# Kernel optimization log

Hardware: AMD Instinct MI355X
Metric: run time of the kernel (lower is better)

The kernel has to match this reference:

```python
import jax, jax.numpy as jnp
import numpy as np

N_NODES = 100000
N_EDGES = 3200000
HIDDEN = 128


def _linear_params(key, din, dout):
    s = 1.0 / np.sqrt(din)
    kw, kb = jax.random.split(key)
    W = jax.random.uniform(kw, (dout, din), minval=-s, maxval=s, dtype=jnp.float32)
    b = jax.random.uniform(kb, (dout,), minval=-s, maxval=s, dtype=jnp.float32)
    return W, b


def setup_inputs() -> dict:
    key = jax.random.key(0)
    ks = jax.random.split(key, 9)
    x = jax.random.normal(ks[0], (N_NODES, 5), dtype=jnp.float32)
    edge_index = jax.random.randint(ks[1], (2, N_EDGES), 0, N_NODES, dtype=jnp.int64)
    W1, b1 = _linear_params(ks[2], 5, 64)
    W2, b2 = _linear_params(ks[3], 64, HIDDEN)
    W3, b3 = _linear_params(ks[4], HIDDEN, HIDDEN)
    W4, b4 = _linear_params(ks[5], HIDDEN, HIDDEN)
    Wc1, bc1 = _linear_params(ks[6], HIDDEN, HIDDEN)
    Wc2, bc2 = _linear_params(ks[7], HIDDEN, HIDDEN)
    W5, b5 = _linear_params(ks[8], HIDDEN, 60)
    return {"x": x, "edge_index": edge_index,
            "W1": W1, "b1": b1, "W2": W2, "b2": b2,
            "W3": W3, "b3": b3, "W4": W4, "b4": b4,
            "Wc1": Wc1, "bc1": bc1, "Wc2": Wc2, "bc2": bc2,
            "W5": W5, "b5": b5}


def gcn_conv(x, edge_index, W, b):
    """GCNConv: self-loops + symmetric deg^-1/2 normalization."""
    n = x.shape[0]
    loop = jnp.arange(n, dtype=edge_index.dtype)
    src = jnp.concatenate([edge_index[0], loop])  # [E+N]
    dst = jnp.concatenate([edge_index[1], loop])  # [E+N]
    h = x @ W.T                                    # [N, H]
    ones = jnp.ones_like(dst, dtype=h.dtype)
    deg = jax.ops.segment_sum(ones, dst, num_segments=n)         # [N]
    dinv = jnp.where(deg > 0, jax.lax.rsqrt(deg), 0.0)
    norm = dinv[src] * dinv[dst]                                  # [E+N]
    msg = h[src] * norm[:, None]                                  # gather + scale
    out = jax.ops.segment_sum(msg, dst, num_segments=n)           # scatter-add
    return out + b


def reference(x, edge_index, W1, b1, W2, b2, W3, b3, W4, b4,
              Wc1, bc1, Wc2, bc2, W5, b5):
    h = jax.nn.relu(x @ W1.T + b1)
    h = jax.nn.relu(h @ W2.T + b2)
    h = jax.nn.relu(h @ W3.T + b3) + h
    h = jax.nn.relu(h @ W4.T + b4) + h
    h = jax.nn.relu(gcn_conv(h, edge_index, Wc1, bc1))
    h = jax.nn.relu(gcn_conv(h, edge_index, Wc2, bc2))
    return h @ W5.T + b5  # [N, 60]
```

## Files before the change

### kernel.cpp

```cpp
#include <hip/hip_runtime.h>
#include <hip/hip_fp16.h>

typedef __attribute__((ext_vector_type(8))) short bf16x8;
typedef __attribute__((ext_vector_type(4))) float f32x4;

__device__ __forceinline__ float frelu(float v){ return fmaxf(v, 0.f); }
__device__ __forceinline__ short f2bf(float f){
  unsigned u = __float_as_uint(f);
  unsigned r = (u + 0x7fffu + ((u>>16)&1u)) >> 16;
  return (short)r;
}
__device__ __forceinline__ float bf2f(short h){
  return __uint_as_float(((unsigned)(unsigned short)h) << 16);
}

template<int K, int BN, int COLS_REAL, int PRE, int EPI, int WRG, int WCG>
__global__ __launch_bounds__(512) void k_mgemm(const float* __restrict__ A,
    const float* __restrict__ W, const float* __restrict__ bpre,
    const float* __restrict__ bpost, const float* __restrict__ dscale,
    float* __restrict__ Out, int n)
{
  constexpr int BM = WRG*64;
  __shared__ __align__(16) short sAh[BM*32];
  __shared__ __align__(16) short sAl[BM*32];
  __shared__ __align__(16) short sWh[BN*32];
  __shared__ __align__(16) short sWl[BN*32];

  const int tid = threadIdx.x;
  const int nb0 = blockIdx.x * BM;
  const int l = tid & 63;
  const int w = tid >> 6;
  const int wr = w % WRG;
  const int wc = w / WRG;
  const int lrow = l & 15;
  const int koct = l >> 4;

  f32x4 acc[4][4];
  #pragma unroll
  for (int i=0;i<4;i++)
    #pragma unroll
    for (int j=0;j<4;j++) acc[i][j] = (f32x4){0.f,0.f,0.f,0.f};

  for (int kc = 0; kc < K/32; ++kc) {
    if (kc) __syncthreads();
    #pragma unroll
    for (int t = 0; t < BM/128; ++t) {
      int idx = tid + t*512;
      int row = idx >> 2, kq = idx & 3;
      int node = nb0 + row;
      float a[8];
      if (node < n) {
        const float* g = A + (size_t)node*K + kc*32 + kq*8;
        float4 v0 = *(const float4*)g;
        float4 v1 = *(const float4*)(g+4);
        a[0]=v0.x; a[1]=v0.y; a[2]=v0.z; a[3]=v0.w;
        a[4]=v1.x; a[5]=v1.y; a[6]=v1.z; a[7]=v1.w;
      } else {
        #pragma unroll
        for (int j=0;j<8;j++) a[j]=0.f;
      }
      if constexpr (PRE == 1) {
        const float* bp = bpre + kc*32 + kq*8;
        float4 b0 = *(const float4*)bp;
        float4 b1 = *(const float4*)(bp+4);
        a[0]=frelu(a[0]+b0.x); a[1]=frelu(a[1]+b0.y);
        a[2]=frelu(a[2]+b0.z); a[3]=frelu(a[3]+b0.w);
        a[4]=frelu(a[4]+b1.x); a[5]=frelu(a[5]+b1.y);
        a[6]=frelu(a[6]+b1.z); a[7]=frelu(a[7]+b1.w);
      }
      union { short s[8]; bf16x8 v; } ph, pl;
      #pragma unroll
      for (int j=0;j<8;j++) {
        short h = f2bf(a[j]);
        ph.s[j] = h;
        pl.s[j] = f2bf(a[j] - bf2f(h));
      }
      int byte = (row<<6) | (kq<<4);
      byte ^= (row&7)<<4;
      *(bf16x8*)((char*)sAh + byte) = ph.v;
      *(bf16x8*)((char*)sAl + byte) = pl.v;
    }
    if (BN*4 >= 512 || tid < BN*4) {
      int idx = tid;
      int c = idx >> 2, kq = idx & 3;
      float a[8];
      if (COLS_REAL == BN || c < COLS_REAL) {
        const float* g = W + (size_t)c*K + kc*32 + kq*8;
        float4 v0 = *(const float4*)g;
        float4 v1 = *(const float4*)(g+4);
        a[0]=v0.x; a[1]=v0.y; a[2]=v0.z; a[3]=v0.w;
        a[4]=v1.x; a[5]=v1.y; a[6]=v1.z; a[7]=v1.w;
      } else {
        #pragma unroll
        for (int j=0;j<8;j++) a[j]=0.f;
      }
      union { short s[8]; bf16x8 v; } ph, pl;
      #pragma unroll
      for (int j=0;j<8;j++) {
        short h = f2bf(a[j]);
        ph.s[j] = h;
        pl.s[j] = f2bf(a[j] - bf2f(h));
      }
      int byte = (c<<6) | (kq<<4);
      byte ^= (c&7)<<4;
      *(bf16x8*)((char*)sWh + byte) = ph.v;
      *(bf16x8*)((char*)sWl + byte) = pl.v;
    }
    __syncthreads();
    bf16x8 fah[4], fal[4], fwh[4], fwl[4];
    #pragma unroll
    for (int rf=0; rf<4; ++rf) {
      int row = wr*64 + rf*16 + lrow;
      int byte = (row<<6) | (koct<<4);
      byte ^= (row&7)<<4;
      fah[rf] = *(const bf16x8*)((const char*)sAh + byte);
      fal[rf] = *(const bf16x8*)((const char*)sAl + byte);
    }
    #pragma unroll
    for (int cf=0; cf<4; ++cf) {
      int c = wc*64 + cf*16 + lrow;
      int byte = (c<<6) | (koct<<4);
      byte ^= (c&7)<<4;
      fwh[cf] = *(const bf16x8*)((const char*)sWh + byte);
      fwl[cf] = *(const bf16x8*)((const char*)sWl + byte);
    }
    #pragma unroll
    for (int rf=0; rf<4; ++rf)
      #pragma unroll
      for (int cf=0; cf<4; ++cf) {
        acc[rf][cf] = __builtin_amdgcn_mfma_f32_16x16x32_bf16(fah[rf], fwh[cf], acc[rf][cf], 0,0,0);
        acc[rf][cf] = __builtin_amdgcn_mfma_f32_16x16x32_bf16(fah[rf], fwl[cf], acc[rf][cf], 0,0,0);
        acc[rf][cf] = __builtin_amdgcn_mfma_f32_16x16x32_bf16(fal[rf], fwh[cf], acc[rf][cf], 0,0,0);
      }
  }
  const int crow = (l >> 4) * 4;
  float bpc[4];
  if constexpr (EPI==1 || EPI==2 || EPI==3) {
    #pragma unroll
    for (int cf=0; cf<4; ++cf) {
      int col = wc*64 + cf*16 + (l & 15);
      bpc[cf] = (COLS_REAL == BN || col < COLS_REAL) ? bpost[col] : 0.f;
    }
  }
  #pragma unroll
  for (int rf=0; rf<4; ++rf) {
    #pragma unroll
    for (int reg=0; reg<4; ++reg) {
      int row = wr*64 + rf*16 + crow + reg;
      int node = nb0 + row;
      if (node >= n) continue;
      float ds = 1.f;
      if constexpr (EPI==4 || EPI==5) ds = dscale[node];
      #pragma unroll
      for (int cf=0; cf<4; ++cf) {
        int col = wc*64 + cf*16 + (l & 15);
        if (COLS_REAL != BN && col >= COLS_REAL) continue;
        float v = acc[rf][cf][reg];
        if constexpr (EPI==1) v += bpc[cf];
        if constexpr (EPI==2) v = frelu(v + bpc[cf]);
        if constexpr (EPI==3) v = frelu(v + bpc[cf]) + A[(size_t)node*K + col];
        if constexpr (EPI==4) v *= ds;
        if constexpr (EPI==5) {
          v *= ds;
          ((__half*)Out)[(size_t)node*COLS_REAL + col] = __float2half_rn(v);
        } else {
          Out[(size_t)node*COLS_REAL + col] = v;
        }
      }
    }
  }
}

__global__ __launch_bounds__(256) void k_wsplit(const float* __restrict__ W2,
    const float* __restrict__ W3, const float* __restrict__ W4,
    const float* __restrict__ Wc1, short* __restrict__ whi, short* __restrict__ wlo)
{
  int idx = blockIdx.x*256 + threadIdx.x;
  if (idx >= 57344) return;
  const float* src; int e, c, k, cbase;
  if (idx < 8192){ src=W2; e=idx; c=e>>6; k=e&63; cbase=0; }
  else if (idx < 24576){ src=W3; e=idx-8192; c=e>>7; k=e&127; cbase=8192; }
  else if (idx < 40960){ src=W4; e=idx-24576; c=e>>7; k=e&127; cbase=24576; }
  else { src=Wc1; e=idx-40960; c=e>>7; k=e&127; cbase=40960; }
  float v = src[e];
  short h = f2bf(v);
  short lo = f2bf(v - bf2f(h));
  int byte = ((c<<6) | ((k&31)<<1)) ^ ((c&7)<<4);
  int pos = cbase + (k>>5)*4096 + (byte>>1);
  whi[pos] = h; wlo[pos] = lo;
}

__global__ __launch_bounds__(256) void k_mega(const float* __restrict__ x,
    const float* __restrict__ W1, const float* __restrict__ b1,
    const float* __restrict__ b2, const float* __restrict__ b3,
    const float* __restrict__ b4, const short* __restrict__ whi,
    const short* __restrict__ wlo, const float* __restrict__ dinv,
    __half* __restrict__ tp1, int n)
{
  __shared__ __align__(16) short sWh[4096], sWl[4096];
  __shared__ __align__(16) short bAh[4096], bAl[4096];
  __shared__ __align__(16) short bBh[4096], bBl[4096];
  __shared__ float sx[160];
  __shared__ float sW1[320];
  __shared__ float sb1[64];
  const int tid = threadIdx.x;
  const int nb0 = blockIdx.x*32;

  if (tid < 160){ int row = tid/5, col = tid - row*5; int node = nb0 + row;
    sx[tid] = (node < n) ? x[(size_t)node*5 + col] : 0.f; }
  if (tid < 64) sb1[tid] = b1[tid];
  for (int i = tid; i < 320; i += 256) sW1[i] = W1[i];
  __syncthreads();

  {
    int row = tid >> 3, c0 = (tid & 7)*8;
    float xr[5];
    #pragma unroll
    for (int k=0;k<5;k++) xr[k] = sx[row*5+k];
    #pragma unroll
    for (int j=0;j<8;j++){
      int c = c0 + j;
      float a = sb1[c];
      #pragma unroll
      for (int k=0;k<5;k++) a = fmaf(xr[k], sW1[c*5+k], a);
      a = frelu(a);
      short h = f2bf(a), lo = f2bf(a - bf2f(h));
      int byte = ((c>>5)<<11) + ((((row<<6)|((c&31)<<1))) ^ ((row&7)<<4));
      *(short*)((char*)bAh + byte) = h;
      *(short*)((char*)bAl + byte) = lo;
    }
  }

  const int l = tid & 63, w = tid >> 6;
  const int wr = w >> 1, wc = w & 1;
  const int lrow = l & 15, koct = l >> 4;
  const int arow = wr*16 + lrow;
  const int abyteNoKc = ((arow<<6)|(koct<<4)) ^ ((arow&7)<<4);
  int wbyte[4];
  #pragma unroll
  for (int cf=0; cf<4; ++cf){
    int c = wc*64 + cf*16 + lrow;
    wbyte[cf] = ((c<<6)|(koct<<4)) ^ ((c&7)<<4);
  }
  f32x4 acc[4];
  float res[4][4];

  auto run_layer = [&](const short* inH, const short* inL, int woff, int nkc){
    #pragma unroll
    for (int cf=0; cf<4; ++cf) acc[cf] = (f32x4){0.f,0.f,0.f,0.f};
    for (int kc=0; kc<nkc; ++kc){
      __syncthreads();
      {
        const bf16x8* gh = (const bf16x8*)(whi + woff + kc*4096);
        const bf16x8* gl = (const bf16x8*)(wlo + woff + kc*4096);
        ((bf16x8*)sWh)[tid*2]   = gh[tid*2];
        ((bf16x8*)sWh)[tid*2+1] = gh[tid*2+1];
        ((bf16x8*)sWl)[tid*2]   = gl[tid*2];
        ((bf16x8*)sWl)[tid*2+1] = gl[tid*2+1];
      }
      __syncthreads();
      int ab = (kc<<11) + abyteNoKc;
      bf16x8 fah = *(const bf16x8*)((const char*)inH + ab);
      bf16x8 fal = *(const bf16x8*)((const char*)inL + ab);
      #pragma unroll
      for (int cf=0; cf<4; ++cf){
        bf16x8 fwh = *(const bf16x8*)((const char*)sWh + wbyte[cf]);
        bf16x8 fwl = *(const bf16x8*)((const char*)sWl + wbyte[cf]);
        acc[cf] = __builtin_amdgcn_mfma_f32_16x16x32_bf16(fah, fwh, acc[cf], 0,0,0);
        acc[cf] = __builtin_amdgcn_mfma_f32_16x16x32_bf16(fah, fwl, acc[cf], 0,0,0);
        acc[cf] = __builtin_amdgcn_mfma_f32_16x16x32_bf16(fal, fwh, acc[cf], 0,0,0);
      }
    }
  };
  auto store_buf = [&](short* outH, short* outL, int cf, int reg, float v){
    int row = wr*16 + koct*4 + reg;
    int col = wc*64 + cf*16 + lrow;
    short h = f2bf(v), lo = f2bf(v - bf2f(h));
    int byte = ((col>>5)<<11) + (((row<<6)|((col&31)<<1)) ^ ((row&7)<<4));
    *(short*)((char*)outH + byte) = h;
    *(short*)((char*)outL + byte) = lo;
  };

  run_layer(bAh, bAl, 0, 2);
  #pragma unroll
  for (int cf=0; cf<4; ++cf){
    float bb = b2[wc*64 + cf*16 + lrow];
    #pragma unroll
    for (int reg=0; reg<4; ++reg){
      float v = frelu(acc[cf][reg] + bb);
      res[cf][reg] = v;
      store_buf(bBh, bBl, cf, reg, v);
    }
  }
  run_layer(bBh, bBl, 8192, 4);
  #pragma unroll
  for (int cf=0; cf<4; ++cf){
    float bb = b3[wc*64 + cf*16 + lrow];
    #pragma unroll
    for (int reg=0; reg<4; ++reg){
      float v = frelu(acc[cf][reg] + bb) + res[cf][reg];
      res[cf][reg] = v;
      store_buf(bAh, bAl, cf, reg, v);
    }
  }
  run_layer(bAh, bAl, 24576, 4);
  #pragma unroll
  for (int cf=0; cf<4; ++cf){
    float bb = b4[wc*64 + cf*16 + lrow];
    #pragma unroll
    for (int reg=0; reg<4; ++reg){
      float v = frelu(acc[cf][reg] + bb) + res[cf][reg];
      store_buf(bBh, bBl, cf, reg, v);
    }
  }
  run_layer(bBh, bBl, 40960, 4);
  #pragma unroll
  for (int reg=0; reg<4; ++reg){
    int row = wr*16 + koct*4 + reg;
    int node = nb0 + row;
    float di = dinv[min(node, n-1)];
    #pragma unroll
    for (int cf=0; cf<4; ++cf){
      int col = wc*64 + cf*16 + lrow;
      if (node < n) tp1[(size_t)node*128 + col] = __float2half_rn(acc[cf][reg]*di);
    }
  }
}

__global__ __launch_bounds__(512) void k_zero512(int* __restrict__ a, int m){
  int i = threadIdx.x; if (i<m) a[i]=0;
}
__global__ __launch_bounds__(512) void k_bhist(const int* __restrict__ dst,
    int* __restrict__ bcnt, int E, int nbuck){
  __shared__ int l[512];
  int tid = threadIdx.x;
  if (tid < nbuck) l[tid]=0;
  __syncthreads();
  for (int e = blockIdx.x*512 + tid; e < E; e += gridDim.x*512)
    atomicAdd(&l[((unsigned)dst[e])>>8], 1);
  __syncthreads();
  if (tid < nbuck && l[tid]) atomicAdd(&bcnt[tid], l[tid]);
}
__global__ __launch_bounds__(512) void k_bscan(const int* __restrict__ bcnt,
    int* __restrict__ bbase, int* __restrict__ bcur, int nbuck){
  __shared__ int sc[512];
  int tid = threadIdx.x;
  int v = (tid<nbuck) ? bcnt[tid] : 0;
  sc[tid]=v; __syncthreads();
  for (int off=1; off<512; off<<=1){
    int t = (tid>=off)? sc[tid-off] : 0;
    __syncthreads();
    sc[tid]+=t;
    __syncthreads();
  }
  if (tid<nbuck){ bbase[tid]=sc[tid]-v; bcur[tid]=sc[tid]-v; }
  if (tid==nbuck-1) bbase[nbuck]=sc[tid];
}
__global__ __launch_bounds__(512) void k_bscatter(const int* __restrict__ src,
    const int* __restrict__ dst, int* __restrict__ bcur,
    unsigned* __restrict__ sorted, int E, int nbuck)
{
  __shared__ int lcnt[512];
  __shared__ int lbase[512];
  int tid = threadIdx.x;
  if (tid < nbuck) lcnt[tid]=0;
  __syncthreads();
  int e0 = blockIdx.x*8192;
  int e1 = min(e0+8192, E);
  for (int e = e0+tid; e < e1; e += 512)
    atomicAdd(&lcnt[((unsigned)dst[e])>>8], 1);
  __syncthreads();
  if (tid < nbuck) lbase[tid] = lcnt[tid] ? atomicAdd(&bcur[tid], lcnt[tid]) : 0;
  __syncthreads();
  if (tid < nbuck) lcnt[tid]=0;
  __syncthreads();
  for (int e = e0+tid; e < e1; e += 512){
    int d = dst[e];
    int k = ((unsigned)d)>>8;
    int pos = lbase[k] + atomicAdd(&lcnt[k], 1);
    sorted[pos] = (((unsigned)src[e])<<8) | ((unsigned)d & 255u);
  }
}
__global__ __launch_bounds__(512) void k_finesort(unsigned* __restrict__ sorted,
    const int* __restrict__ bbase, int* __restrict__ cend,
    float* __restrict__ dinv, int n, int* __restrict__ fb)
{
  constexpr int CAP = 16384;
  __shared__ int lsorted[CAP];
  __shared__ int cnt[256], cur[256], sc[256];
  const int k = blockIdx.x;
  const int base = bbase[k], endb = bbase[k+1];
  const int m = endb - base;
  const int node0 = k<<8;
  const int tid = threadIdx.x;
  if (tid<256) cnt[tid]=0;
  __syncthreads();
  for (int i=tid; i<m; i+=512) atomicAdd(&cnt[sorted[base+i]&255u], 1);
  __syncthreads();
  int v=0;
  if (tid<256){ v=cnt[tid]; sc[tid]=v; }
  __syncthreads();
  for (int off=1; off<256; off<<=1){
    int t=0;
    if (tid>=off && tid<256) t=sc[tid-off];
    __syncthreads();
    if (tid<256) sc[tid]+=t;
    __syncthreads();
  }
  if (tid<256){
    cur[tid]=sc[tid]-v;
    int node = node0 + tid;
    if (node < n){
      cend[node] = base + sc[tid];
      dinv[node] = rsqrtf((float)v + 1.0f);
    }
  }
  __syncthreads();
  if (m <= CAP){
    for (int i=tid; i<m; i+=512){
      unsigned p = sorted[base+i];
      int pos = atomicAdd(&cur[p&255u], 1);
      lsorted[pos] = (int)(p>>8);
    }
    __syncthreads();
    for (int i=tid; i<m; i+=512) sorted[base+i] = (unsigned)lsorted[i];
  } else {
    for (int i=tid; i<m; i+=512) fb[base+i] = (int)sorted[base+i];
    __syncthreads();
    for (int i=tid; i<m; i+=512){
      unsigned p = (unsigned)fb[base+i];
      int pos = atomicAdd(&cur[p&255u], 1);
      sorted[base+pos] = p>>8;
    }
  }
}

__global__ __launch_bounds__(256) void k_agg(const int* __restrict__ cend,
    const unsigned* __restrict__ srcs, const float* __restrict__ dinv,
    const __half* __restrict__ tp, float* __restrict__ out, int n)
{
  int node = blockIdx.x*4 + (threadIdx.x>>6);
  if (node >= n) return;
  const int lane = threadIdx.x & 63;
  const __half2* tpp = (const __half2*)tp;
  int beg = (node==0) ? 0 : cend[node-1];
  int end = cend[node];
  float2 acc;
  { __half2 h = tpp[(size_t)node*64 + lane]; acc.x = __low2float(h); acc.y = __high2float(h); }
  int e = beg;
  for (; e+4<=end; e+=4){
    unsigned s0=srcs[e], s1=srcs[e+1], s2=srcs[e+2], s3=srcs[e+3];
    __half2 h0 = tpp[(size_t)s0*64 + lane];
    __half2 h1 = tpp[(size_t)s1*64 + lane];
    __half2 h2 = tpp[(size_t)s2*64 + lane];
    __half2 h3 = tpp[(size_t)s3*64 + lane];
    acc.x += (__low2float(h0)+__low2float(h1)) + (__low2float(h2)+__low2float(h3));
    acc.y += (__high2float(h0)+__high2float(h1)) + (__high2float(h2)+__high2float(h3));
  }
  for (; e<end; ++e){
    __half2 h = tpp[(size_t)srcs[e]*64 + lane];
    acc.x += __low2float(h); acc.y += __high2float(h);
  }
  float di = dinv[node];
  float2 r; r.x = acc.x*di; r.y = acc.y*di;
  *(float2*)(out + (size_t)node*128 + (lane<<1)) = r;
}

extern "C" void kernel_launch(void* const* d_in, const int* in_sizes, int n_in,
                              void* d_out, int out_size, void* d_ws, size_t ws_size,
                              hipStream_t stream)
{
  const float* x   = (const float*)d_in[0];
  const int*   ei  = (const int*)d_in[1];
  const float *W1=(const float*)d_in[2],  *b1=(const float*)d_in[3];
  const float *W2=(const float*)d_in[4],  *b2=(const float*)d_in[5];
  const float *W3=(const float*)d_in[6],  *b3=(const float*)d_in[7];
  const float *W4=(const float*)d_in[8],  *b4=(const float*)d_in[9];
  const float *Wc1=(const float*)d_in[10],*bc1=(const float*)d_in[11];
  const float *Wc2=(const float*)d_in[12],*bc2=(const float*)d_in[13];
  const float *W5=(const float*)d_in[14], *b5=(const float*)d_in[15];
  float* out = (float*)d_out;

  const int n = in_sizes[0] / 5;
  const int E = in_sizes[1] / 2;
  const int* esrc = ei;
  const int* edst = ei + E;
  const int nbuck = (n + 255) >> 8;

  dim3 B256(256), B512(512);
  const int G256 = (n + 255)/256;
  const int G512 = (n + 511)/512;

  char* p = (char*)d_ws;
  float* hA    = (float*)p;           p += (size_t)n*128*4;
  float* hB    = (float*)p;           p += (size_t)n*128*4;
  float* dinv  = (float*)p;           p += (size_t)n*4;
  int*   cend  = (int*)p;             p += (size_t)n*4;
  unsigned* sortedp = (unsigned*)p;   p += (size_t)E*4;
  int*   bcnt  = (int*)p;             p += 512*4;
  int*   bbase = (int*)p;             p += 513*4;
  int*   bcur  = (int*)p;             p += 512*4;
  short* whi   = (short*)p;           p += 57344*2;
  short* wlo   = (short*)p;           p += 57344*2;

  k_zero512<<<dim3(1), B512, 0, stream>>>(bcnt, nbuck);
  k_bhist<<<dim3(512), B512, 0, stream>>>(edst, bcnt, E, nbuck);
  k_bscan<<<dim3(1), B512, 0, stream>>>(bcnt, bbase, bcur, nbuck);
  k_bscatter<<<dim3((E + 8191)/8192), B512, 0, stream>>>(esrc, edst, bcur, sortedp, E, nbuck);
  k_finesort<<<dim3(nbuck), B512, 0, stream>>>(sortedp, bbase, cend, dinv, n, (int*)hA);

  k_wsplit<<<dim3(224), B256, 0, stream>>>(W2, W3, W4, Wc1, whi, wlo);

  k_mega<<<dim3((n + 31)/32), B256, 0, stream>>>(x, W1, b1, b2, b3, b4,
                                                 whi, wlo, dinv, (__half*)hA, n);
  k_agg<<<dim3((n+3)/4), B256, 0, stream>>>(cend, sortedp, dinv, (const __half*)hA, hB, n);

  k_mgemm<128,128,128,1,5,4,2><<<dim3(G256), B512, 0, stream>>>(hB, Wc2, bc1, nullptr, dinv, hA, n);
  k_agg<<<dim3((n+3)/4), B256, 0, stream>>>(cend, sortedp, dinv, (const __half*)hA, hB, n);

  k_mgemm<128,64,60,1,1,8,1><<<dim3(G512), B512, 0, stream>>>(hB, W5, bc2, b5, nullptr, out, n);
}
```

Before: 448.8 us.

## Store transformed features column-chunked and aggregate per 16-column chunk

The fp16 transformed features are now written in a chunk-major layout: 8 chunks of 16 columns, each stored contiguously across all nodes. The aggregation kernel gives each block one column chunk, so a chunk's gather working set is about 3.2 MB instead of the full 25.6 MB table, which should raise L2 hit rates. Within a wavefront, 8 edges are processed in parallel with 8 lanes per edge, and a shuffle reduction follows. In exchange, each gathered row segment is only 32 bytes, edge indices are re-read once per chunk (8x), and the tail iterations use masked loads.

After: 1.006 ms. 2.24x slower.

```diff
diff --git a/kernel.cpp b/kernel.cpp
--- a/kernel.cpp
+++ b/kernel.cpp
@@ -162,7 +162,7 @@
         if constexpr (EPI==4) v *= ds;
         if constexpr (EPI==5) {
           v *= ds;
-          ((__half*)Out)[(size_t)node*COLS_REAL + col] = __float2half_rn(v);
+          ((__half*)Out)[((size_t)(col>>4)*n + node)*16 + (col&15)] = __float2half_rn(v);
         } else {
           Out[(size_t)node*COLS_REAL + col] = v;
         }
@@ -322,7 +322,8 @@
     #pragma unroll
     for (int cf=0; cf<4; ++cf){
       int col = wc*64 + cf*16 + lrow;
-      if (node < n) tp1[(size_t)node*128 + col] = __float2half_rn(acc[cf][reg]*di);
+      if (node < n)
+        tp1[((size_t)(col>>4)*n + node)*16 + (col&15)] = __float2half_rn(acc[cf][reg]*di);
     }
   }
 }
@@ -435,35 +436,42 @@
   }
 }
 
-__global__ __launch_bounds__(256) void k_agg(const int* __restrict__ cend,
+__global__ __launch_bounds__(512) void k_aggc(const int* __restrict__ cend,
     const unsigned* __restrict__ srcs, const float* __restrict__ dinv,
     const __half* __restrict__ tp, float* __restrict__ out, int n)
 {
-  int node = blockIdx.x*4 + (threadIdx.x>>6);
+  const int chunk = blockIdx.x & 7;
+  const int node = (blockIdx.x >> 3)*8 + (threadIdx.x >> 6);
   if (node >= n) return;
-  const int lane = threadIdx.x & 63;
-  const __half2* tpp = (const __half2*)tp;
-  int beg = (node==0) ? 0 : cend[node-1];
-  int end = cend[node];
-  float2 acc;
-  { __half2 h = tpp[(size_t)node*64 + lane]; acc.x = __low2float(h); acc.y = __high2float(h); }
-  int e = beg;
-  for (; e+4<=end; e+=4){
-    unsigned s0=srcs[e], s1=srcs[e+1], s2=srcs[e+2], s3=srcs[e+3];
-    __half2 h0 = tpp[(size_t)s0*64 + lane];
-    __half2 h1 = tpp[(size_t)s1*64 + lane];
-    __half2 h2 = tpp[(size_t)s2*64 + lane];
-    __half2 h3 = tpp[(size_t)s3*64 + lane];
-    acc.x += (__low2float(h0)+__low2float(h1)) + (__low2float(h2)+__low2float(h3));
-    acc.y += (__high2float(h0)+__high2float(h1)) + (__high2float(h2)+__high2float(h3));
-  }
-  for (; e<end; ++e){
-    __half2 h = tpp[(size_t)srcs[e]*64 + lane];
+  const int l = threadIdx.x & 63;
+  const int eg = l >> 3, ch = l & 7;
+  const __half2* tpc = (const __half2*)tp + (size_t)chunk*n*8;
+  const int beg = (node==0) ? 0 : cend[node-1];
+  const int end = cend[node];
+  float2 acc = {0.f, 0.f};
+  const int iters = (end - beg + 7) >> 3;
+  for (int i=0; i<iters; ++i){
+    int e = beg + i*8 + eg;
+    int ec = min(e, end-1);
+    unsigned s = __builtin_nontemporal_load(srcs + ec);
+    __half2 h = tpc[(size_t)s*8 + ch];
+    float m = (e < end) ? 1.f : 0.f;
+    acc.x = fmaf(__low2float(h), m, acc.x);
+    acc.y = fmaf(__high2float(h), m, acc.y);
+  }
+  #pragma unroll
+  for (int msk=8; msk<64; msk<<=1){
+    acc.x += __shfl_xor(acc.x, msk, 64);
+    acc.y += __shfl_xor(acc.y, msk, 64);
+  }
+  if (eg == 0){
+    __half2 h = tpc[(size_t)node*8 + ch];
     acc.x += __low2float(h); acc.y += __high2float(h);
-  }
-  float di = dinv[node];
-  float2 r; r.x = acc.x*di; r.y = acc.y*di;
-  *(float2*)(out + (size_t)node*128 + (lane<<1)) = r;
+    float di = dinv[node];
+    float2 r; r.x = acc.x*di; r.y = acc.y*di;
+    double rb; __builtin_memcpy(&rb, &r, 8);
+    __builtin_nontemporal_store(rb, (double*)(out + (size_t)node*128 + (chunk*8+ch)*2));
+  }
 }
 
 extern "C" void kernel_launch(void* const* d_in, const int* in_sizes, int n_in,
@@ -490,6 +498,7 @@
   dim3 B256(256), B512(512);
   const int G256 = (n + 255)/256;
   const int G512 = (n + 511)/512;
+  const int GAGG = 8 * ((n + 7)/8);
 
   char* p = (char*)d_ws;
   float* hA    = (float*)p;           p += (size_t)n*128*4;
@@ -513,10 +522,10 @@
 
   k_mega<<<dim3((n + 31)/32), B256, 0, stream>>>(x, W1, b1, b2, b3, b4,
                                                  whi, wlo, dinv, (__half*)hA, n);
-  k_agg<<<dim3((n+3)/4), B256, 0, stream>>>(cend, sortedp, dinv, (const __half*)hA, hB, n);
+  k_aggc<<<dim3(GAGG), B512, 0, stream>>>(cend, sortedp, dinv, (const __half*)hA, hB, n);
 
   k_mgemm<128,128,128,1,5,4,2><<<dim3(G256), B512, 0, stream>>>(hB, Wc2, bc1, nullptr, dinv, hA, n);
-  k_agg<<<dim3((n+3)/4), B256, 0, stream>>>(cend, sortedp, dinv, (const __half*)hA, hB, n);
+  k_aggc<<<dim3(GAGG), B512, 0, stream>>>(cend, sortedp, dinv, (const __half*)hA, hB, n);
 
   k_mgemm<128,64,60,1,1,8,1><<<dim3(G512), B512, 0, stream>>>(hB, W5, bc2, b5, nullptr, out, n);
 }
```

## Fuse GCN aggregation with following dense GEMM into one kernel

Applied to the files above, without the earlier changes.

Replaces the separate aggregation kernel and split-bf16 GEMM pair with a single kernel. Each 512-thread block gathers neighbour rows for 128 nodes, applies the dinv scale, bias and ReLU, and writes the result as hi/lo bf16 into shared memory. It then runs the MFMA GEMM directly on that tile. This removes the fp32 round trip of the aggregated features through global memory. The cost is a large shared-memory tile that limits occupancy for the latency-bound gather phase, and the GEMM cannot start until the whole block's gather is done.

Measured after the change: 631.5 us. 1.41x slower.

```diff
diff --git a/kernel.cpp b/kernel.cpp
--- a/kernel.cpp
+++ b/kernel.cpp
@@ -12,163 +12,6 @@
 }
 __device__ __forceinline__ float bf2f(short h){
   return __uint_as_float(((unsigned)(unsigned short)h) << 16);
-}
-
-template<int K, int BN, int COLS_REAL, int PRE, int EPI, int WRG, int WCG>
-__global__ __launch_bounds__(512) void k_mgemm(const float* __restrict__ A,
-    const float* __restrict__ W, const float* __restrict__ bpre,
-    const float* __restrict__ bpost, const float* __restrict__ dscale,
-    float* __restrict__ Out, int n)
-{
-  constexpr int BM = WRG*64;
-  __shared__ __align__(16) short sAh[BM*32];
-  __shared__ __align__(16) short sAl[BM*32];
-  __shared__ __align__(16) short sWh[BN*32];
-  __shared__ __align__(16) short sWl[BN*32];
-
-  const int tid = threadIdx.x;
-  const int nb0 = blockIdx.x * BM;
-  const int l = tid & 63;
-  const int w = tid >> 6;
-  const int wr = w % WRG;
-  const int wc = w / WRG;
-  const int lrow = l & 15;
-  const int koct = l >> 4;
-
-  f32x4 acc[4][4];
-  #pragma unroll
-  for (int i=0;i<4;i++)
-    #pragma unroll
-    for (int j=0;j<4;j++) acc[i][j] = (f32x4){0.f,0.f,0.f,0.f};
-
-  for (int kc = 0; kc < K/32; ++kc) {
-    if (kc) __syncthreads();
-    #pragma unroll
-    for (int t = 0; t < BM/128; ++t) {
-      int idx = tid + t*512;
-      int row = idx >> 2, kq = idx & 3;
-      int node = nb0 + row;
-      float a[8];
-      if (node < n) {
-        const float* g = A + (size_t)node*K + kc*32 + kq*8;
-        float4 v0 = *(const float4*)g;
-        float4 v1 = *(const float4*)(g+4);
-        a[0]=v0.x; a[1]=v0.y; a[2]=v0.z; a[3]=v0.w;
-        a[4]=v1.x; a[5]=v1.y; a[6]=v1.z; a[7]=v1.w;
-      } else {
-        #pragma unroll
-        for (int j=0;j<8;j++) a[j]=0.f;
-      }
-      if constexpr (PRE == 1) {
-        const float* bp = bpre + kc*32 + kq*8;
-        float4 b0 = *(const float4*)bp;
-        float4 b1 = *(const float4*)(bp+4);
-        a[0]=frelu(a[0]+b0.x); a[1]=frelu(a[1]+b0.y);
-        a[2]=frelu(a[2]+b0.z); a[3]=frelu(a[3]+b0.w);
-        a[4]=frelu(a[4]+b1.x); a[5]=frelu(a[5]+b1.y);
-        a[6]=frelu(a[6]+b1.z); a[7]=frelu(a[7]+b1.w);
-      }
-      union { short s[8]; bf16x8 v; } ph, pl;
-      #pragma unroll
-      for (int j=0;j<8;j++) {
-        short h = f2bf(a[j]);
-        ph.s[j] = h;
-        pl.s[j] = f2bf(a[j] - bf2f(h));
-      }
-      int byte = (row<<6) | (kq<<4);
-      byte ^= (row&7)<<4;
-      *(bf16x8*)((char*)sAh + byte) = ph.v;
-      *(bf16x8*)((char*)sAl + byte) = pl.v;
-    }
-    if (BN*4 >= 512 || tid < BN*4) {
-      int idx = tid;
-      int c = idx >> 2, kq = idx & 3;
-      float a[8];
-      if (COLS_REAL == BN || c < COLS_REAL) {
-        const float* g = W + (size_t)c*K + kc*32 + kq*8;
-        float4 v0 = *(const float4*)g;
-        float4 v1 = *(const float4*)(g+4);
-        a[0]=v0.x; a[1]=v0.y; a[2]=v0.z; a[3]=v0.w;
-        a[4]=v1.x; a[5]=v1.y; a[6]=v1.z; a[7]=v1.w;
-      } else {
-        #pragma unroll
-        for (int j=0;j<8;j++) a[j]=0.f;
-      }
-      union { short s[8]; bf16x8 v; } ph, pl;
-      #pragma unroll
-      for (int j=0;j<8;j++) {
-        short h = f2bf(a[j]);
-        ph.s[j] = h;
-        pl.s[j] = f2bf(a[j] - bf2f(h));
-      }
-      int byte = (c<<6) | (kq<<4);
-      byte ^= (c&7)<<4;
-      *(bf16x8*)((char*)sWh + byte) = ph.v;
-      *(bf16x8*)((char*)sWl + byte) = pl.v;
-    }
-    __syncthreads();
-    bf16x8 fah[4], fal[4], fwh[4], fwl[4];
-    #pragma unroll
-    for (int rf=0; rf<4; ++rf) {
-      int row = wr*64 + rf*16 + lrow;
-      int byte = (row<<6) | (koct<<4);
-      byte ^= (row&7)<<4;
-      fah[rf] = *(const bf16x8*)((const char*)sAh + byte);
-      fal[rf] = *(const bf16x8*)((const char*)sAl + byte);
-    }
-    #pragma unroll
-    for (int cf=0; cf<4; ++cf) {
-      int c = wc*64 + cf*16 + lrow;
-      int byte = (c<<6) | (koct<<4);
-      byte ^= (c&7)<<4;
-      fwh[cf] = *(const bf16x8*)((const char*)sWh + byte);
-      fwl[cf] = *(const bf16x8*)((const char*)sWl + byte);
-    }
-    #pragma unroll
-    for (int rf=0; rf<4; ++rf)
-      #pragma unroll
-      for (int cf=0; cf<4; ++cf) {
-        acc[rf][cf] = __builtin_amdgcn_mfma_f32_16x16x32_bf16(fah[rf], fwh[cf], acc[rf][cf], 0,0,0);
-        acc[rf][cf] = __builtin_amdgcn_mfma_f32_16x16x32_bf16(fah[rf], fwl[cf], acc[rf][cf], 0,0,0);
-        acc[rf][cf] = __builtin_amdgcn_mfma_f32_16x16x32_bf16(fal[rf], fwh[cf], acc[rf][cf], 0,0,0);
-      }
-  }
-  const int crow = (l >> 4) * 4;
-  float bpc[4];
-  if constexpr (EPI==1 || EPI==2 || EPI==3) {
-    #pragma unroll
-    for (int cf=0; cf<4; ++cf) {
-      int col = wc*64 + cf*16 + (l & 15);
-      bpc[cf] = (COLS_REAL == BN || col < COLS_REAL) ? bpost[col] : 0.f;
-    }
-  }
-  #pragma unroll
-  for (int rf=0; rf<4; ++rf) {
-    #pragma unroll
-    for (int reg=0; reg<4; ++reg) {
-      int row = wr*64 + rf*16 + crow + reg;
-      int node = nb0 + row;
-      if (node >= n) continue;
-      float ds = 1.f;
-      if constexpr (EPI==4 || EPI==5) ds = dscale[node];
-      #pragma unroll
-      for (int cf=0; cf<4; ++cf) {
-        int col = wc*64 + cf*16 + (l & 15);
-        if (COLS_REAL != BN && col >= COLS_REAL) continue;
-        float v = acc[rf][cf][reg];
-        if constexpr (EPI==1) v += bpc[cf];
-        if constexpr (EPI==2) v = frelu(v + bpc[cf]);
-        if constexpr (EPI==3) v = frelu(v + bpc[cf]) + A[(size_t)node*K + col];
-        if constexpr (EPI==4) v *= ds;
-        if constexpr (EPI==5) {
-          v *= ds;
-          ((__half*)Out)[(size_t)node*COLS_REAL + col] = __float2half_rn(v);
-        } else {
-          Out[(size_t)node*COLS_REAL + col] = v;
-        }
-      }
-    }
-  }
 }
 
 __global__ __launch_bounds__(256) void k_wsplit(const float* __restrict__ W2,
@@ -322,7 +165,8 @@
     #pragma unroll
     for (int cf=0; cf<4; ++cf){
       int col = wc*64 + cf*16 + lrow;
-      if (node < n) tp1[(size_t)node*128 + col] = __float2half_rn(acc[cf][reg]*di);
+      if (node < n)
+        tp1[(size_t)node*128 + col] = __float2half_rn(acc[cf][reg]*di);
     }
   }
 }
@@ -435,35 +279,157 @@
   }
 }
 
-__global__ __launch_bounds__(256) void k_agg(const int* __restrict__ cend,
-    const unsigned* __restrict__ srcs, const float* __restrict__ dinv,
-    const __half* __restrict__ tp, float* __restrict__ out, int n)
-{
-  int node = blockIdx.x*4 + (threadIdx.x>>6);
-  if (node >= n) return;
-  const int lane = threadIdx.x & 63;
+template<int BN, int COLS_REAL, int WCG, int EPI>
+__global__ __launch_bounds__(512) void k_gagg(const __half* __restrict__ tp,
+    const int* __restrict__ cend, const unsigned* __restrict__ srcs,
+    const float* __restrict__ dinv, const float* __restrict__ bpre,
+    const float* __restrict__ W, const float* __restrict__ bpost,
+    void* __restrict__ Outv, int n)
+{
+  constexpr int WRG = 8/WCG;
+  constexpr int RF  = 8/WRG;
+  __shared__ __align__(16) short sAh[16384], sAl[16384];
+  __shared__ __align__(16) short sWh[BN*32], sWl[BN*32];
+  const int tid = threadIdx.x;
+  const int w = tid >> 6, l = tid & 63;
+  const int nb0 = blockIdx.x*128;
   const __half2* tpp = (const __half2*)tp;
-  int beg = (node==0) ? 0 : cend[node-1];
-  int end = cend[node];
-  float2 acc;
-  { __half2 h = tpp[(size_t)node*64 + lane]; acc.x = __low2float(h); acc.y = __high2float(h); }
-  int e = beg;
-  for (; e+4<=end; e+=4){
-    unsigned s0=srcs[e], s1=srcs[e+1], s2=srcs[e+2], s3=srcs[e+3];
-    __half2 h0 = tpp[(size_t)s0*64 + lane];
-    __half2 h1 = tpp[(size_t)s1*64 + lane];
-    __half2 h2 = tpp[(size_t)s2*64 + lane];
-    __half2 h3 = tpp[(size_t)s3*64 + lane];
-    acc.x += (__low2float(h0)+__low2float(h1)) + (__low2float(h2)+__low2float(h3));
-    acc.y += (__high2float(h0)+__high2float(h1)) + (__high2float(h2)+__high2float(h3));
-  }
-  for (; e<end; ++e){
-    __half2 h = tpp[(size_t)srcs[e]*64 + lane];
-    acc.x += __low2float(h); acc.y += __high2float(h);
-  }
-  float di = dinv[node];
-  float2 r; r.x = acc.x*di; r.y = acc.y*di;
-  *(float2*)(out + (size_t)node*128 + (lane<<1)) = r;
+
+  const float bcx = bpre[2*l], bcy = bpre[2*l+1];
+  for (int i=0; i<16; ++i){
+    const int r = w + (i<<3);
+    const int node = nb0 + r;
+    float2 acc = {0.f, 0.f};
+    if (node < n){
+      const int beg = (node==0) ? 0 : cend[node-1];
+      const int end = cend[node];
+      __half2 h = tpp[(size_t)node*64 + l];
+      acc.x = __low2float(h); acc.y = __high2float(h);
+      int e = beg;
+      for (; e+4<=end; e+=4){
+        unsigned s0=srcs[e], s1=srcs[e+1], s2=srcs[e+2], s3=srcs[e+3];
+        __half2 h0 = tpp[(size_t)s0*64 + l];
+        __half2 h1 = tpp[(size_t)s1*64 + l];
+        __half2 h2 = tpp[(size_t)s2*64 + l];
+        __half2 h3 = tpp[(size_t)s3*64 + l];
+        acc.x += (__low2float(h0)+__low2float(h1)) + (__low2float(h2)+__low2float(h3));
+        acc.y += (__high2float(h0)+__high2float(h1)) + (__high2float(h2)+__high2float(h3));
+      }
+      for (; e<end; ++e){
+        __half2 hh = tpp[(size_t)srcs[e]*64 + l];
+        acc.x += __low2float(hh); acc.y += __high2float(hh);
+      }
+      const float di = dinv[node];
+      acc.x = frelu(fmaf(acc.x, di, bcx));
+      acc.y = frelu(fmaf(acc.y, di, bcy));
+    }
+    union { short s[2]; unsigned u; } ph, pl;
+    ph.s[0] = f2bf(acc.x); pl.s[0] = f2bf(acc.x - bf2f(ph.s[0]));
+    ph.s[1] = f2bf(acc.y); pl.s[1] = f2bf(acc.y - bf2f(ph.s[1]));
+    const int k = l << 1;
+    const int byte = ((k>>5)<<13) + ((((r<<6)|((k&31)<<1))) ^ ((r&7)<<4));
+    *(unsigned*)((char*)sAh + byte) = ph.u;
+    *(unsigned*)((char*)sAl + byte) = pl.u;
+  }
+  __syncthreads();
+
+  const int wr = w % WRG, wc = w / WRG;
+  const int lrow = l & 15, koct = l >> 4;
+  f32x4 acc[RF][4];
+  #pragma unroll
+  for (int rf=0; rf<RF; ++rf)
+    #pragma unroll
+    for (int cf=0; cf<4; ++cf) acc[rf][cf] = (f32x4){0.f,0.f,0.f,0.f};
+  int abyte[RF], wbyte[4];
+  #pragma unroll
+  for (int rf=0; rf<RF; ++rf){
+    int arow = wr*(RF*16) + rf*16 + lrow;
+    abyte[rf] = ((arow<<6)|(koct<<4)) ^ ((arow&7)<<4);
+  }
+  #pragma unroll
+  for (int cf=0; cf<4; ++cf){
+    int c = wc*64 + cf*16 + lrow;
+    wbyte[cf] = ((c<<6)|(koct<<4)) ^ ((c&7)<<4);
+  }
+  for (int kc=0; kc<4; ++kc){
+    if (kc) __syncthreads();
+    if (BN*4 >= 512 || tid < BN*4){
+      int c = tid >> 2, kq = tid & 3;
+      float a[8];
+      if (COLS_REAL == BN || c < COLS_REAL){
+        const float* g = W + (size_t)c*128 + kc*32 + kq*8;
+        float4 v0 = *(const float4*)g;
+        float4 v1 = *(const float4*)(g+4);
+        a[0]=v0.x; a[1]=v0.y; a[2]=v0.z; a[3]=v0.w;
+        a[4]=v1.x; a[5]=v1.y; a[6]=v1.z; a[7]=v1.w;
+      } else {
+        #pragma unroll
+        for (int j=0;j<8;j++) a[j]=0.f;
+      }
+      union { short s[8]; bf16x8 v; } ph, pl;
+      #pragma unroll
+      for (int j=0;j<8;j++){
+        short h = f2bf(a[j]);
+        ph.s[j] = h;
+        pl.s[j] = f2bf(a[j] - bf2f(h));
+      }
+      int byte = ((c<<6)|(kq<<4)) ^ ((c&7)<<4);
+      *(bf16x8*)((char*)sWh + byte) = ph.v;
+      *(bf16x8*)((char*)sWl + byte) = pl.v;
+    }
+    __syncthreads();
+    bf16x8 fah[RF], fal[RF], fwh[4], fwl[4];
+    #pragma unroll
+    for (int rf=0; rf<RF; ++rf){
+      int ab = (kc<<13) + abyte[rf];
+      fah[rf] = *(const bf16x8*)((const char*)sAh + ab);
+      fal[rf] = *(const bf16x8*)((const char*)sAl + ab);
+    }
+    #pragma unroll
+    for (int cf=0; cf<4; ++cf){
+      fwh[cf] = *(const bf16x8*)((const char*)sWh + wbyte[cf]);
+      fwl[cf] = *(const bf16x8*)((const char*)sWl + wbyte[cf]);
+    }
+    #pragma unroll
+    for (int rf=0; rf<RF; ++rf)
+      #pragma unroll
+      for (int cf=0; cf<4; ++cf){
+        acc[rf][cf] = __builtin_amdgcn_mfma_f32_16x16x32_bf16(fah[rf], fwh[cf], acc[rf][cf], 0,0,0);
+        acc[rf][cf] = __builtin_amdgcn_mfma_f32_16x16x32_bf16(fah[rf], fwl[cf], acc[rf][cf], 0,0,0);
+        acc[rf][cf] = __builtin_amdgcn_mfma_f32_16x16x32_bf16(fal[rf], fwh[cf], acc[rf][cf], 0,0,0);
+      }
+  }
+  const int crow = koct*4;
+  float bpc[4];
+  if constexpr (EPI == 1){
+    #pragma unroll
+    for (int cf=0; cf<4; ++cf){
+      int col = wc*64 + cf*16 + lrow;
+      bpc[cf] = (COLS_REAL == BN || col < COLS_REAL) ? bpost[col] : 0.f;
+    }
+  }
+  #pragma unroll
+  for (int rf=0; rf<RF; ++rf){
+    #pragma unroll
+    for (int reg=0; reg<4; ++reg){
+      int row = wr*(RF*16) + rf*16 + crow + reg;
+      int node = nb0 + row;
+      if (node >= n) continue;
+      float ds = 1.f;
+      if constexpr (EPI == 5) ds = dinv[node];
+      #pragma unroll
+      for (int cf=0; cf<4; ++cf){
+        int col = wc*64 + cf*16 + lrow;
+        if (COLS_REAL != BN && col >= COLS_REAL) continue;
+        float v = acc[rf][cf][reg];
+        if constexpr (EPI == 5){
+          ((__half*)Outv)[(size_t)node*128 + col] = __float2half_rn(v*ds);
+        } else {
+          ((float*)Outv)[(size_t)node*COLS_REAL + col] = v + bpc[cf];
+        }
+      }
+    }
+  }
 }
 
 extern "C" void kernel_launch(void* const* d_in, const int* in_sizes, int n_in,
@@ -488,8 +454,7 @@
   const int nbuck = (n + 255) >> 8;
 
   dim3 B256(256), B512(512);
-  const int G256 = (n + 255)/256;
-  const int G512 = (n + 511)/512;
+  const int G128 = (n + 127)/128;
 
   char* p = (char*)d_ws;
   float* hA    = (float*)p;           p += (size_t)n*128*4;
@@ -513,10 +478,10 @@
 
   k_mega<<<dim3((n + 31)/32), B256, 0, stream>>>(x, W1, b1, b2, b3, b4,
                                                  whi, wlo, dinv, (__half*)hA, n);
-  k_agg<<<dim3((n+3)/4), B256, 0, stream>>>(cend, sortedp, dinv, (const __half*)hA, hB, n);
-
-  k_mgemm<128,128,128,1,5,4,2><<<dim3(G256), B512, 0, stream>>>(hB, Wc2, bc1, nullptr, dinv, hA, n);
-  k_agg<<<dim3((n+3)/4), B256, 0, stream>>>(cend, sortedp, dinv, (const __half*)hA, hB, n);
-
-  k_mgemm<128,64,60,1,1,8,1><<<dim3(G512), B512, 0, stream>>>(hB, W5, bc2, b5, nullptr, out, n);
-}
+
+  k_gagg<128,128,2,5><<<dim3(G128), B512, 0, stream>>>((const __half*)hA, cend, sortedp,
+      dinv, bc1, Wc2, nullptr, hB, n);
+
+  k_gagg<64,60,1,1><<<dim3(G128), B512, 0, stream>>>((const __half*)hB, cend, sortedp,
+      dinv, bc2, W5, b5, out, n);
+}
```
